# Kernel optimization log

Measured on AMD Instinct MI355X. Metric: run time of the kernel, lower is better.

## Reference

```python
import jax, jax.numpy as jnp
import numpy as np

N = 50000        # nodes per type (MiRNA=0, Disease=1, LncRNA=2)
E = 500000       # edges per relation
F_IN, HID, OUT = 128, 64, 64
ITEMS, SIZE, T = 4096, 4096, 100
# relation order: MvsD, DvsM, MvsL, LvsM, LvsD, DvsL
SRC = (0, 1, 0, 2, 2, 1)
DST = (1, 0, 2, 0, 1, 2)


def _sage_hetero_layer(h, edges, Wp, bp, Ws, bs, Wn):
    """One HeteroGraphConv(SAGEConv pool, aggregate='sum') layer.
    h: list of 3 [N, Fin] node-feature arrays; edges: [6, 2, E] int."""
    n = h[0].shape[0]
    out = [None, None, None]
    for e in range(6):
        s, d = SRC[e], DST[e]
        pooled = jax.nn.relu(h[s] @ Wp[e] + bp[e])                 # [N, Fin]
        msg = pooled[edges[e, 0]]                                  # [E, Fin] gather at src
        agg = jax.ops.segment_max(msg, edges[e, 1], num_segments=n)
        agg = jnp.where(jnp.isneginf(agg), 0.0, agg)               # DGL: 0 for isolated dst
        o = h[d] @ Ws[e] + bs[e] + agg @ Wn[e]                     # fc_self(+bias) + fc_neigh
        out[d] = o if out[d] is None else out[d] + o
    return out


def setup_inputs() -> dict:
    key = jax.random.key(0)
    ks = jax.random.split(key, 32)
    s = 0.05
    inp = {
        'hM': jax.random.normal(ks[0], (N, F_IN), jnp.float32),
        'hD': jax.random.normal(ks[1], (N, F_IN), jnp.float32),
        'hL': jax.random.normal(ks[2], (N, F_IN), jnp.float32),
        'Wpool1': jax.random.normal(ks[3], (6, F_IN, F_IN), jnp.float32) * s,
        'bpool1': jnp.zeros((6, F_IN), jnp.float32),
        'Wself1': jax.random.normal(ks[4], (6, F_IN, HID), jnp.float32) * s,
        'bself1': jnp.zeros((6, HID), jnp.float32),
        'Wneigh1': jax.random.normal(ks[5], (6, F_IN, HID), jnp.float32) * s,
        'Wpool2': jax.random.normal(ks[6], (6, HID, HID), jnp.float32) * s,
        'bpool2': jnp.zeros((6, HID), jnp.float32),
        'Wself2': jax.random.normal(ks[7], (6, HID, HID), jnp.float32) * s,
        'bself2': jnp.zeros((6, HID), jnp.float32),
        'Wneigh2': jax.random.normal(ks[8], (6, HID, HID), jnp.float32) * s,
        'Wpool3': jax.random.normal(ks[9], (6, HID, HID), jnp.float32) * s,
        'bpool3': jnp.zeros((6, HID), jnp.float32),
        'Wself3': jax.random.normal(ks[10], (6, HID, OUT), jnp.float32) * s,
        'bself3': jnp.zeros((6, OUT), jnp.float32),
        'Wneigh3': jax.random.normal(ks[11], (6, HID, OUT), jnp.float32) * s,
        'Adj': jax.random.uniform(ks[12], (SIZE, ITEMS), jnp.float32),
        'noise': jax.random.normal(ks[13], (N, OUT), jnp.float32),
        'W1': jax.random.normal(ks[14], (ITEMS + OUT, 256), jnp.float32) * s,
        'b1': jnp.zeros((256,), jnp.float32),
        'W2': jax.random.normal(ks[15], (256, 512), jnp.float32) * s,
        'b2': jnp.zeros((512,), jnp.float32),
        'W3': jax.random.normal(ks[16], (512, 1024), jnp.float32) * s,
        'b3': jnp.zeros((1024,), jnp.float32),
        'W4': jax.random.normal(ks[17], (1024, ITEMS), jnp.float32) * s,
        'b4': jnp.zeros((ITEMS,), jnp.float32),
        'edges': jax.random.randint(ks[18], (6, 2, E), 0, N, jnp.int32),
        't': 50,
        'size': SIZE,
        'leftIndex': 0,
    }
    return inp


def reference(hM, hD, hL, Wpool1, bpool1, Wself1, bself1, Wneigh1,
              Wpool2, bpool2, Wself2, bself2, Wneigh2,
              Wpool3, bpool3, Wself3, bself3, Wneigh3,
              Adj, noise, W1, b1, W2, b2, W3, b3, W4, b4,
              edges, t, size, leftIndex):
    h1 = _sage_hetero_layer([hM, hD, hL], edges, Wpool1, bpool1, Wself1, bself1, Wneigh1)
    h2 = _sage_hetero_layer(h1, edges, Wpool2, bpool2, Wself2, bself2, Wneigh2)
    h3 = _sage_hetero_layer(h2, edges, Wpool3, bpool3, Wself3, bself3, Wneigh3)
    mirna = h3[0]                                                  # [N, OUT]
    mirna = mirna / jnp.maximum(jnp.sum(jnp.abs(mirna), axis=1, keepdims=True), 1e-12)
    # diffusion schedule
    betas = jnp.linspace(1e-4, 0.02, T, dtype=jnp.float32)
    alpha_bars = jnp.cumprod(1.0 - betas)
    signal_rates = jnp.sqrt(alpha_bars)
    noise_rates = jnp.sqrt(1.0 - alpha_bars)
    noisy = signal_rates[t] * mirna + noise_rates[t] * noise
    fake = jax.lax.stop_gradient(noisy[leftIndex:leftIndex + size])  # detach + slice
    M = jnp.concatenate([Adj, fake], axis=1)                       # [size, ITEMS+OUT]
    x = jax.nn.relu(M @ W1 + b1)
    x = jax.nn.relu(x @ W2 + b2)
    x = jax.nn.relu(x @ W3 + b3)
    x = jax.nn.sigmoid(x @ W4 + b4)
    return fake, x
```

## Files before the change

### kernel.cpp

```cpp
#include <hip/hip_runtime.h>
#include <hip/hip_bf16.h>

#define NNODE 50000
#define NEDGE 500000
#define SZ    4096
#define NBKT  256
#define BWID  196
#define BCAP  4096
#define RELEB ((size_t)NBKT * BCAP)
#define ZK1   8

typedef __attribute__((ext_vector_type(8))) short bf16x8;
typedef __attribute__((ext_vector_type(4))) float f32x4;

__device__ __forceinline__ float bits2f(unsigned short u) {
    return __uint_as_float(((unsigned)u) << 16);
}
__device__ __forceinline__ unsigned short f2bits(float f) {
    unsigned x = __float_as_uint(f);
    unsigned r = x + 0x7fffu + ((x >> 16) & 1u);
    return (unsigned short)(r >> 16);
}
__device__ __forceinline__ unsigned pk_max_u16(unsigned a, unsigned b) {
    unsigned lo = max(a & 0xffffu, b & 0xffffu);
    unsigned hi = max(a >> 16, b >> 16);
    return lo | (hi << 16);
}
__device__ __forceinline__ void gl_lds16(const void* g, void* l) {
    __builtin_amdgcn_global_load_lds(
        (const __attribute__((address_space(1))) unsigned int*)g,
        (__attribute__((address_space(3))) unsigned int*)l, 16, 0, 0);
}

template<int RELU, int SIG, int OUTF32, int PART, int PIPE>
__global__ __launch_bounds__(256)
void gemm128(const unsigned short* __restrict__ A, const unsigned short* __restrict__ Bt,
             const float* __restrict__ bias, void* __restrict__ Cv, int M, int N, int K)
{
    __shared__ unsigned short As[PIPE + 1][128 * 64];
    __shared__ unsigned short Bs[PIPE + 1][128 * 64];
    const int tid = threadIdx.x;
    const int wave = tid >> 6, lane = tid & 63;
    const int m16 = lane & 15, quad = lane >> 4;
    const int wr = wave >> 1, wc = wave & 1;
    const int nwg = gridDim.x * gridDim.y;
    int bid = blockIdx.y * gridDim.x + blockIdx.x;
    if ((nwg & 7) == 0) { int cpx = nwg >> 3; bid = (bid & 7) * cpx + (bid >> 3); }
    const int bx = bid % gridDim.x, by = bid / gridDim.x;
    const int row0 = by * 128, col0 = bx * 128;
    const int lrow = lane >> 3, lcol = (lane & 7) * 8;

    f32x4 acc[4][4] = {};

    int k0beg = 0, k0end = K;
    if (PART) {
        const int per = ((K >> 6) + gridDim.z - 1) / gridDim.z;
        k0beg = blockIdx.z * per * 64;
        k0end = min(K, k0beg + per * 64);
    }
    const int nt = (k0end - k0beg) >> 6;

    auto STAGE = [&](int b, int k0) {
#pragma unroll
        for (int i = 0; i < 4; ++i) {
            int chunk = wave * 4 + i;
            int row = chunk * 8 + lrow;
            gl_lds16(A  + (size_t)(row0 + row) * K + k0 + lcol, &As[b][chunk * 512]);
            gl_lds16(Bt + (size_t)(col0 + row) * K + k0 + lcol, &Bs[b][chunk * 512]);
        }
    };
    auto COMPUTE = [&](int b) {
#pragma unroll
        for (int ks = 0; ks < 2; ++ks) {
            bf16x8 a[4], bb[4];
#pragma unroll
            for (int mt = 0; mt < 4; ++mt)
                a[mt] = *(const bf16x8*)&As[b][(wr * 64 + mt * 16 + m16) * 64 + ks * 32 + quad * 8];
#pragma unroll
            for (int nt2 = 0; nt2 < 4; ++nt2)
                bb[nt2] = *(const bf16x8*)&Bs[b][(wc * 64 + nt2 * 16 + m16) * 64 + ks * 32 + quad * 8];
#pragma unroll
            for (int mt = 0; mt < 4; ++mt)
#pragma unroll
                for (int nt2 = 0; nt2 < 4; ++nt2)
                    acc[mt][nt2] = __builtin_amdgcn_mfma_f32_16x16x32_bf16(a[mt], bb[nt2], acc[mt][nt2], 0, 0, 0);
        }
    };

    if (PIPE) {
        STAGE(0, k0beg);
        __syncthreads();
        int cur = 0;
        for (int t = 0; t < nt; ++t) {
            if (t + 1 < nt) STAGE(cur ^ 1, k0beg + (t + 1) * 64);
            COMPUTE(cur);
            __syncthreads();
            cur ^= 1;
        }
    } else {
        for (int t = 0; t < nt; ++t) {
            STAGE(0, k0beg + t * 64);
            __syncthreads();
            COMPUTE(0);
            __syncthreads();
        }
    }

    if (PART) {
        float* P = (float*)Cv + (size_t)blockIdx.z * M * N;
#pragma unroll
        for (int mt = 0; mt < 4; ++mt)
#pragma unroll
            for (int nt2 = 0; nt2 < 4; ++nt2) {
                int gc = col0 + wc * 64 + nt2 * 16 + m16;
#pragma unroll
                for (int r = 0; r < 4; ++r) {
                    int gm = row0 + wr * 64 + mt * 16 + quad * 4 + r;
                    P[(size_t)gm * N + gc] = acc[mt][nt2][r];
                }
            }
        return;
    }

#pragma unroll
    for (int mt = 0; mt < 4; ++mt) {
#pragma unroll
        for (int nt2 = 0; nt2 < 4; ++nt2) {
            int gc = col0 + wc * 64 + nt2 * 16 + m16;
            float bv = bias[gc];
#pragma unroll
            for (int r = 0; r < 4; ++r) {
                int gm = row0 + wr * 64 + mt * 16 + quad * 4 + r;
                size_t idx = (size_t)gm * N + gc;
                float v = acc[mt][nt2][r] + bv;
                if (RELU) v = fmaxf(v, 0.f);
                if (SIG)  v = 1.f / (1.f + __expf(-v));
                if (OUTF32) ((float*)Cv)[idx] = v;
                else        ((unsigned short*)Cv)[idx] = f2bits(v);
            }
        }
    }
}

__global__ __launch_bounds__(256)
void mlp1_ep_k(const float* __restrict__ p, const float* __restrict__ b1,
               unsigned short* __restrict__ x1)
{
    const size_t MN = (size_t)SZ * 256;
    int i = blockIdx.x * 256 + threadIdx.x;
    if (i >= (int)(MN / 4)) return;
    float4 s = ((const float4*)p)[i];
#pragma unroll
    for (int z = 1; z < ZK1; ++z) {
        float4 a = ((const float4*)(p + (size_t)z * MN))[i];
        s.x += a.x; s.y += a.y; s.z += a.z; s.w += a.w;
    }
    int base = i * 4;
    ushort4 o;
    o.x = f2bits(fmaxf(s.x + b1[(base + 0) & 255], 0.f));
    o.y = f2bits(fmaxf(s.y + b1[(base + 1) & 255], 0.f));
    o.z = f2bits(fmaxf(s.z + b1[(base + 2) & 255], 0.f));
    o.w = f2bits(fmaxf(s.w + b1[(base + 3) & 255], 0.f));
    ((ushort4*)x1)[i] = o;
}

template<int NT>
__global__ __launch_bounds__(256)
void pool2_k(const unsigned short* __restrict__ A0, const unsigned short* __restrict__ A1,
             const unsigned short* __restrict__ Bt0, const unsigned short* __restrict__ Bt1,
             const float* __restrict__ b0, const float* __restrict__ b1,
             unsigned short* __restrict__ out, int M, int K)
{
    __shared__ unsigned short As[64][72];
    __shared__ unsigned short Bs[NT * 16][72];
    const int z = blockIdx.z;
    const unsigned short* A = z ? A1 : A0;
    const unsigned short* Bt = z ? Bt1 : Bt0;
    const float* bias = z ? b1 : b0;
    const int N = NT * 16;
    unsigned short* Cv = out + (size_t)z * M * N;

    const int tid = threadIdx.x;
    const int wave = tid >> 6, lane = tid & 63;
    const int m16 = lane & 15, quad = lane >> 4;
    const int row0 = blockIdx.y * 64, col0 = blockIdx.x * N;

    f32x4 acc[NT] = {};

    for (int k0 = 0; k0 < K; k0 += 64) {
#pragma unroll
        for (int it = 0; it < 2; ++it) {
            int u = tid + it * 256;
            int m = u >> 3, c = (u & 7) * 8;
            int gm = row0 + m;
            uint4 v = make_uint4(0u, 0u, 0u, 0u);
            if (gm < M) v = *(const uint4*)(A + (size_t)gm * K + k0 + c);
            *(uint4*)&As[m][c] = v;
        }
#pragma unroll
        for (int it = 0; it < NT / 2; ++it) {
            int u = tid + it * 256;
            int n = u >> 3, c = (u & 7) * 8;
            uint4 v = *(const uint4*)(Bt + (size_t)(col0 + n) * K + k0 + c);
            *(uint4*)&Bs[n][c] = v;
        }
        __syncthreads();
#pragma unroll
        for (int ks = 0; ks < 2; ++ks) {
            bf16x8 a = *(const bf16x8*)&As[wave * 16 + m16][ks * 32 + quad * 8];
#pragma unroll
            for (int nt = 0; nt < NT; ++nt) {
                bf16x8 b = *(const bf16x8*)&Bs[nt * 16 + m16][ks * 32 + quad * 8];
                acc[nt] = __builtin_amdgcn_mfma_f32_16x16x32_bf16(a, b, acc[nt], 0, 0, 0);
            }
        }
        __syncthreads();
    }

#pragma unroll
    for (int nt = 0; nt < NT; ++nt) {
        int gc = col0 + nt * 16 + m16;
        float bv = bias[gc];
#pragma unroll
        for (int r = 0; r < 4; ++r) {
            int gm = row0 + wave * 16 + quad * 4 + r;
            if (gm < M)
                Cv[(size_t)gm * N + gc] = f2bits(fmaxf(acc[nt][r] + bv, 0.f));
        }
    }
}

__global__ __launch_bounds__(256)
void pool6_k(const unsigned short* __restrict__ hin, const unsigned short* __restrict__ pT,
             const float* __restrict__ bp, unsigned short* __restrict__ pooled6, int M)
{
    const int SRCr[6] = {0, 1, 0, 2, 2, 1};
    __shared__ unsigned short As[64][72];
    __shared__ unsigned short Bs[64][72];
    const int z = blockIdx.z;
    const unsigned short* A = hin + (size_t)SRCr[z] * M * 64;
    const unsigned short* Bt = pT + (size_t)z * 4096;
    const float* bias = bp + z * 64;
    unsigned short* Cv = pooled6 + (size_t)z * M * 64;

    const int tid = threadIdx.x;
    const int wave = tid >> 6, lane = tid & 63;
    const int m16 = lane & 15, quad = lane >> 4;
    const int row0 = blockIdx.y * 64;

    f32x4 acc[4] = {};

    {
#pragma unroll
        for (int it = 0; it < 2; ++it) {
            int u = tid + it * 256;
            int m = u >> 3, c = (u & 7) * 8;
            int gm = row0 + m;
            uint4 v = make_uint4(0u, 0u, 0u, 0u);
            if (gm < M) v = *(const uint4*)(A + (size_t)gm * 64 + c);
            *(uint4*)&As[m][c] = v;
        }
#pragma unroll
        for (int it = 0; it < 2; ++it) {
            int u = tid + it * 256;
            int n = u >> 3, c = (u & 7) * 8;
            uint4 v = *(const uint4*)(Bt + (size_t)n * 64 + c);
            *(uint4*)&Bs[n][c] = v;
        }
        __syncthreads();
#pragma unroll
        for (int ks = 0; ks < 2; ++ks) {
            bf16x8 a = *(const bf16x8*)&As[wave * 16 + m16][ks * 32 + quad * 8];
#pragma unroll
            for (int nt = 0; nt < 4; ++nt) {
                bf16x8 b = *(const bf16x8*)&Bs[nt * 16 + m16][ks * 32 + quad * 8];
                acc[nt] = __builtin_amdgcn_mfma_f32_16x16x32_bf16(a, b, acc[nt], 0, 0, 0);
            }
        }
    }

#pragma unroll
    for (int nt = 0; nt < 4; ++nt) {
        int gc = nt * 16 + m16;
        float bv = bias[gc];
#pragma unroll
        for (int r = 0; r < 4; ++r) {
            int gm = row0 + wave * 16 + quad * 4 + r;
            if (gm < M)
                Cv[(size_t)gm * 64 + gc] = f2bits(fmaxf(acc[nt][r] + bv, 0.f));
        }
    }
}

template<int NT>
__global__ __launch_bounds__(256)
void mfma_gemm(const unsigned short* __restrict__ A1, const unsigned short* __restrict__ A2,
               const unsigned short* __restrict__ A3,
               const unsigned short* __restrict__ Bt, const float* __restrict__ bias,
               const float* __restrict__ bias2,
               unsigned short* __restrict__ Cv, int M, int N, int Ka, int Kb, int Kc)
{
    __shared__ unsigned short As[64][72];
    __shared__ unsigned short Bs[NT * 16][72];
    const int tid = threadIdx.x;
    const int wave = tid >> 6, lane = tid & 63;
    const int m16 = lane & 15, quad = lane >> 4;
    const int row0 = blockIdx.y * 64, col0 = blockIdx.x * (NT * 16);
    const int K = Ka + Kb + Kc;

    f32x4 acc[NT] = {};

    for (int k0 = 0; k0 < K; k0 += 64) {
        const int seg = (k0 >= Ka + Kb) ? 2 : ((k0 >= Ka) ? 1 : 0);
        const unsigned short* src = seg == 2 ? A3 : (seg == 1 ? A2 : A1);
        const int ld = seg == 2 ? Kc : (seg == 1 ? Kb : Ka);
        const int kb = k0 - (seg == 2 ? Ka + Kb : (seg == 1 ? Ka : 0));
#pragma unroll
        for (int it = 0; it < 2; ++it) {
            int u = tid + it * 256;
            int m = u >> 3, c = (u & 7) * 8;
            int gm = row0 + m;
            uint4 v = make_uint4(0u, 0u, 0u, 0u);
            if (gm < M) v = *(const uint4*)(src + (size_t)gm * ld + kb + c);
            *(uint4*)&As[m][c] = v;
        }
#pragma unroll
        for (int it = 0; it < NT / 2; ++it) {
            int u = tid + it * 256;
            int n = u >> 3, c = (u & 7) * 8;
            uint4 v = *(const uint4*)(Bt + (size_t)(col0 + n) * K + k0 + c);
            *(uint4*)&Bs[n][c] = v;
        }
        __syncthreads();
#pragma unroll
        for (int ks = 0; ks < 2; ++ks) {
            bf16x8 a = *(const bf16x8*)&As[wave * 16 + m16][ks * 32 + quad * 8];
#pragma unroll
            for (int nt = 0; nt < NT; ++nt) {
                bf16x8 b = *(const bf16x8*)&Bs[nt * 16 + m16][ks * 32 + quad * 8];
                acc[nt] = __builtin_amdgcn_mfma_f32_16x16x32_bf16(a, b, acc[nt], 0, 0, 0);
            }
        }
        __syncthreads();
    }

#pragma unroll
    for (int nt = 0; nt < NT; ++nt) {
        int gc = col0 + nt * 16 + m16;
        float bv = bias[gc] + bias2[gc];
#pragma unroll
        for (int r = 0; r < 4; ++r) {
            int gm = row0 + wave * 16 + quad * 4 + r;
            if (gm < M)
                Cv[(size_t)gm * N + gc] = f2bits(acc[nt][r] + bv);
        }
    }
}

__global__ __launch_bounds__(256)
void fused3_k(const unsigned short* __restrict__ hin,
              const unsigned short* __restrict__ regA, const unsigned short* __restrict__ regB,
              const unsigned short* __restrict__ fT, const float* __restrict__ bs,
              unsigned short* __restrict__ hout, int M)
{
    const int PAe[3] = {1, 0, 2}, PBe[3] = {3, 4, 5};
    __shared__ unsigned short As[64][72];
    __shared__ unsigned short Bs[64][72];
    const int z = blockIdx.z;
    const int eA = PAe[z], eB = PBe[z];
    const unsigned short* A1 = hin + (size_t)z * M * 64;
    const unsigned short* A2 = (eA < 4) ? regA + (size_t)eA * M * 64 : regB + (size_t)(eA - 4) * M * 64;
    const unsigned short* A3 = (eB < 4) ? regA + (size_t)eB * M * 64 : regB + (size_t)(eB - 4) * M * 64;
    const unsigned short* Bt = fT + (size_t)z * 12288;
    const float* bias = bs + eA * 64;
    const float* bias2 = bs + eB * 64;
    unsigned short* Cv = hout + (size_t)z * M * 64;

    const int tid = threadIdx.x;
    const int wave = tid >> 6, lane = tid & 63;
    const int m16 = lane & 15, quad = lane >> 4;
    const int row0 = blockIdx.y * 64;

    f32x4 acc[4] = {};

#pragma unroll
    for (int seg = 0; seg < 3; ++seg) {
        const unsigned short* src = seg == 2 ? A3 : (seg == 1 ? A2 : A1);
        const int k0 = seg * 64;
#pragma unroll
        for (int it = 0; it < 2; ++it) {
            int u = tid + it * 256;
            int m = u >> 3, c = (u & 7) * 8;
            int gm = row0 + m;
            uint4 v = make_uint4(0u, 0u, 0u, 0u);
            if (gm < M) v = *(const uint4*)(src + (size_t)gm * 64 + c);
            *(uint4*)&As[m][c] = v;
        }
#pragma unroll
        for (int it = 0; it < 2; ++it) {
            int u = tid + it * 256;
            int n = u >> 3, c = (u & 7) * 8;
            uint4 v = *(const uint4*)(Bt + (size_t)n * 192 + k0 + c);
            *(uint4*)&Bs[n][c] = v;
        }
        __syncthreads();
#pragma unroll
        for (int ks = 0; ks < 2; ++ks) {
            bf16x8 a = *(const bf16x8*)&As[wave * 16 + m16][ks * 32 + quad * 8];
#pragma unroll
            for (int nt = 0; nt < 4; ++nt) {
                bf16x8 b = *(const bf16x8*)&Bs[nt * 16 + m16][ks * 32 + quad * 8];
                acc[nt] = __builtin_amdgcn_mfma_f32_16x16x32_bf16(a, b, acc[nt], 0, 0, 0);
            }
        }
        __syncthreads();
    }

#pragma unroll
    for (int nt = 0; nt < 4; ++nt) {
        int gc = nt * 16 + m16;
        float bv = bias[gc] + bias2[gc];
#pragma unroll
        for (int r = 0; r < 4; ++r) {
            int gm = row0 + wave * 16 + quad * 4 + r;
            if (gm < M)
                Cv[(size_t)gm * 64 + gc] = f2bits(acc[nt][r] + bv);
        }
    }
}

__global__ __launch_bounds__(256)
void transpose_cvt(const float* __restrict__ src1, const float* __restrict__ src2,
                   unsigned short* __restrict__ dst, int R1, int R2, int Nn)
{
    __shared__ float tile[32][33];
    const int R = R1 + R2;
    const int e = blockIdx.z;
    src1 += (size_t)e * R1 * Nn;
    if (src2) src2 += (size_t)e * R2 * Nn;
    dst += (size_t)e * Nn * R;
    const int r0 = blockIdx.x * 32, n0 = blockIdx.y * 32;
    const int lr = threadIdx.x >> 5, ln = threadIdx.x & 31;
#pragma unroll
    for (int i = 0; i < 4; ++i) {
        int r = r0 + lr + i * 8, n = n0 + ln;
        float v = 0.f;
        if (r < R && n < Nn) v = (r < R1) ? src1[(size_t)r * Nn + n]
                                          : src2[(size_t)(r - R1) * Nn + n];
        tile[lr + i * 8][ln] = v;
    }
    __syncthreads();
#pragma unroll
    for (int i = 0; i < 4; ++i) {
        int n = n0 + lr + i * 8, r = r0 + ln;
        if (n < Nn && r < R) dst[(size_t)n * R + r] = f2bits(tile[ln][lr + i * 8]);
    }
}

__global__ __launch_bounds__(256)
void fuse_w_k(const float* __restrict__ Ws, const float* __restrict__ Wn,
              unsigned short* __restrict__ dst, int F)
{
    const int PAe[3] = {1, 0, 2}, PBe[3] = {3, 4, 5};
    __shared__ float tile[32][33];
    const int p = blockIdx.z;
    const int eA = PAe[p], eB = PBe[p];
    const int Kt = 3 * F;
    unsigned short* D = dst + (size_t)p * 64 * Kt;
    const int r0 = blockIdx.x * 32;
    const int n0 = blockIdx.y * 32;
    const int lr = threadIdx.x >> 5, ln = threadIdx.x & 31;
    for (int seg = 0; seg < 3; ++seg) {
        __syncthreads();
#pragma unroll
        for (int i = 0; i < 4; ++i) {
            int r = r0 + lr + i * 8, n = n0 + ln;
            float v;
            if (seg == 0)
                v = Ws[((size_t)eA * F + r) * 64 + n] + Ws[((size_t)eB * F + r) * 64 + n];
            else if (seg == 1)
                v = Wn[((size_t)eA * F + r) * 64 + n];
            else
                v = Wn[((size_t)eB * F + r) * 64 + n];
            tile[lr + i * 8][ln] = v;
        }
        __syncthreads();
        const int koff = seg * F;
#pragma unroll
        for (int i = 0; i < 4; ++i) {
            int n = n0 + lr + i * 8, r = r0 + ln;
            D[(size_t)n * Kt + koff + r] = f2bits(tile[ln][lr + i * 8]);
        }
    }
}

__global__ __launch_bounds__(256)
void cvt3_k(const float* __restrict__ s0, const float* __restrict__ s1,
            const float* __restrict__ s2, unsigned short* __restrict__ dst)
{
    const int z = blockIdx.z;
    const float* src = z == 0 ? s0 : (z == 1 ? s1 : s2);
    dst += (size_t)z * NNODE * 128;
    int i = blockIdx.x * 256 + threadIdx.x;
    if (i >= 1600000) return;
    float4 v = ((const float4*)src)[i];
    ushort4 w;
    w.x = f2bits(v.x); w.y = f2bits(v.y); w.z = f2bits(v.z); w.w = f2bits(v.w);
    ((ushort4*)dst)[i] = w;
}

__global__ __launch_bounds__(256)
void cvt_adj_k(const float* __restrict__ src, unsigned short* __restrict__ dst)
{
    int i = blockIdx.x * 256 + threadIdx.x;
    if (i >= 4194304) return;
    int r = i >> 10, c4 = i & 1023;
    float4 v = ((const float4*)src)[i];
    ushort4 w;
    w.x = f2bits(v.x); w.y = f2bits(v.y); w.z = f2bits(v.z); w.w = f2bits(v.w);
    *(ushort4*)(dst + (size_t)r * 4160 + c4 * 4) = w;
}

__global__ __launch_bounds__(256)
void binit_k(int* __restrict__ bcur)
{
    bcur[blockIdx.x * NBKT + threadIdx.x] = threadIdx.x * BCAP;
}

__global__ __launch_bounds__(256)
void bucket_k(const int* __restrict__ edges, int* __restrict__ bcur,
              unsigned* __restrict__ ebuf)
{
    const int r = blockIdx.y;
    const int base = blockIdx.x * 4096;
    const int tid = threadIdx.x;
    __shared__ int lcnt[NBKT];
    __shared__ int lbase[NBKT];
    for (int i = tid; i < NBKT; i += 256) lcnt[i] = 0;
    __syncthreads();
    unsigned ent[16];
    int rnk[16];
#pragma unroll
    for (int i = 0; i < 16; ++i) {
        int e = base + tid + i * 256;
        ent[i] = 0xffffffffu;
        rnk[i] = 0;
        if (e < NEDGE) {
            int src = edges[(size_t)r * 2 * NEDGE + e];
            int dst = edges[(size_t)r * 2 * NEDGE + NEDGE + e];
            ent[i] = ((unsigned)dst << 16) | (unsigned)src;
            rnk[i] = atomicAdd(&lcnt[dst / BWID], 1);
        }
    }
    __syncthreads();
    for (int i = tid; i < NBKT; i += 256)
        lbase[i] = lcnt[i] ? atomicAdd(&bcur[r * NBKT + i], lcnt[i]) : 0;
    __syncthreads();
#pragma unroll
    for (int i = 0; i < 16; ++i)
        if (ent[i] != 0xffffffffu) {
            int b = (int)(ent[i] >> 16) / BWID;
            int pos = lbase[b] + rnk[i];
            if (pos < (b + 1) * BCAP)
                ebuf[(size_t)r * RELEB + pos] = ent[i];
        }
}

__global__ __launch_bounds__(256)
void bscan_k(const int* __restrict__ bcur, int* __restrict__ bbase,
             int* __restrict__ offs)
{
    const int r = blockIdx.x, tid = threadIdx.x;
    const int lane = tid & 63, wv = tid >> 6;
    int v = bcur[r * NBKT + tid] - tid * BCAP;
    if (v > BCAP) v = BCAP;
    int x = v;
#pragma unroll
    for (int off = 1; off < 64; off <<= 1) {
        int t = __shfl_up(x, off);
        if (lane >= off) x += t;
    }
    __shared__ int wsum[4];
    if (lane == 63) wsum[wv] = x;
    __syncthreads();
    int add = 0;
#pragma unroll
    for (int w = 0; w < 4; ++w) if (w < wv) add += wsum[w];
    x += add;
    bbase[r * NBKT + tid] = x - v;
    if (tid == 255) offs[(size_t)r * (NNODE + 1) + NNODE] = x;
}

__global__ __launch_bounds__(256)
void debucket_k(const unsigned* __restrict__ ebuf, const int* __restrict__ bcur,
                const int* __restrict__ bbase, int* __restrict__ offs,
                unsigned short* __restrict__ srcs)
{
    const int r = blockIdx.y, b = blockIdx.x, tid = threadIdx.x;
    const int lo = b * BWID;
    __shared__ unsigned es[BCAP];
    __shared__ unsigned short stage[BCAP];
    __shared__ int lhist[256];
    __shared__ int buf[256];
    __shared__ int lcur[256];
    int cnt = bcur[r * NBKT + b] - b * BCAP;
    if (cnt > BCAP) cnt = BCAP;
    const int base = bbase[r * NBKT + b];
    lhist[tid] = 0;
    __syncthreads();
    for (int j = tid; j < cnt; j += 256) {
        unsigned e = ebuf[(size_t)r * RELEB + (size_t)b * BCAP + j];
        es[j] = e;
        atomicAdd(&lhist[(int)(e >> 16) - lo], 1);
    }
    __syncthreads();
    int v = lhist[tid];
    buf[tid] = v;
    __syncthreads();
    for (int off = 1; off < 256; off <<= 1) {
        int t = (tid >= off) ? buf[tid - off] : 0;
        __syncthreads();
        buf[tid] += t;
        __syncthreads();
    }
    int excl = buf[tid] - v;
    int node = lo + tid;
    if (tid < BWID && node < NNODE) offs[(size_t)r * (NNODE + 1) + node] = base + excl;
    lcur[tid] = excl;
    __syncthreads();
    for (int j = tid; j < cnt; j += 256) {
        unsigned e = es[j];
        int d = (int)(e >> 16) - lo;
        int p = atomicAdd(&lcur[d], 1);
        stage[p] = (unsigned short)(e & 0xffffu);
    }
    __syncthreads();
    for (int j = tid; j < cnt; j += 256)
        srcs[(size_t)r * NEDGE + base + j] = stage[j];
}

template<int F>
__global__ __launch_bounds__(256)
void gather2_k(const unsigned short* __restrict__ pooled, const int* __restrict__ offs,
               const unsigned short* __restrict__ srcs, unsigned short* __restrict__ agg,
               int e0, int e1)
{
    const int CG = F / 8;
    const int z = blockIdx.z;
    const int e = z ? e1 : e0;
    pooled += (size_t)z * NNODE * F;
    agg    += (size_t)z * NNODE * F;
    offs   += (size_t)e * (NNODE + 1);
    srcs   += (size_t)e * NEDGE;
    int idx = blockIdx.x * 256 + threadIdx.x;
    int n = idx / CG, cg = idx % CG;
    if (n >= NNODE) return;
    int beg = offs[n], end = offs[n + 1];
    unsigned m0 = 0, m1 = 0, m2 = 0, m3 = 0;
    int j = beg;
    for (; j + 4 <= end; j += 4) {
        int s0 = srcs[j], s1 = srcs[j + 1], s2 = srcs[j + 2], s3 = srcs[j + 3];
        uint4 v0 = *(const uint4*)(pooled + (size_t)s0 * F + cg * 8);
        uint4 v1 = *(const uint4*)(pooled + (size_t)s1 * F + cg * 8);
        uint4 v2 = *(const uint4*)(pooled + (size_t)s2 * F + cg * 8);
        uint4 v3 = *(const uint4*)(pooled + (size_t)s3 * F + cg * 8);
        m0 = pk_max_u16(m0, pk_max_u16(pk_max_u16(v0.x, v1.x), pk_max_u16(v2.x, v3.x)));
        m1 = pk_max_u16(m1, pk_max_u16(pk_max_u16(v0.y, v1.y), pk_max_u16(v2.y, v3.y)));
        m2 = pk_max_u16(m2, pk_max_u16(pk_max_u16(v0.z, v1.z), pk_max_u16(v2.z, v3.z)));
        m3 = pk_max_u16(m3, pk_max_u16(pk_max_u16(v0.w, v1.w), pk_max_u16(v2.w, v3.w)));
    }
    for (; j < end; ++j) {
        int s = srcs[j];
        uint4 v = *(const uint4*)(pooled + (size_t)s * F + cg * 8);
        m0 = pk_max_u16(m0, v.x);
        m1 = pk_max_u16(m1, v.y);
        m2 = pk_max_u16(m2, v.z);
        m3 = pk_max_u16(m3, v.w);
    }
    uint4 o; o.x = m0; o.y = m1; o.z = m2; o.w = m3;
    *(uint4*)(agg + (size_t)n * F + cg * 8) = o;
}

__global__ __launch_bounds__(256)
void gather6_k(const unsigned short* __restrict__ pooled6, const int* __restrict__ offs,
               const unsigned short* __restrict__ srcs,
               unsigned short* __restrict__ regA, unsigned short* __restrict__ regB)
{
    const int F = 64, CG = 8;
    const int z = blockIdx.z;
    const unsigned short* pooled = pooled6 + (size_t)z * NNODE * F;
    unsigned short* agg = (z < 4) ? regA + (size_t)z * NNODE * F
                                  : regB + (size_t)(z - 4) * NNODE * F;
    offs += (size_t)z * (NNODE + 1);
    srcs += (size_t)z * NEDGE;
    int idx = blockIdx.x * 256 + threadIdx.x;
    int n = idx / CG, cg = idx % CG;
    if (n >= NNODE) return;
    int beg = offs[n], end = offs[n + 1];
    unsigned m0 = 0, m1 = 0, m2 = 0, m3 = 0;
    int j = beg;
    for (; j + 4 <= end; j += 4) {
        int s0 = srcs[j], s1 = srcs[j + 1], s2 = srcs[j + 2], s3 = srcs[j + 3];
        uint4 v0 = *(const uint4*)(pooled + (size_t)s0 * F + cg * 8);
        uint4 v1 = *(const uint4*)(pooled + (size_t)s1 * F + cg * 8);
        uint4 v2 = *(const uint4*)(pooled + (size_t)s2 * F + cg * 8);
        uint4 v3 = *(const uint4*)(pooled + (size_t)s3 * F + cg * 8);
        m0 = pk_max_u16(m0, pk_max_u16(pk_max_u16(v0.x, v1.x), pk_max_u16(v2.x, v3.x)));
        m1 = pk_max_u16(m1, pk_max_u16(pk_max_u16(v0.y, v1.y), pk_max_u16(v2.y, v3.y)));
        m2 = pk_max_u16(m2, pk_max_u16(pk_max_u16(v0.z, v1.z), pk_max_u16(v2.z, v3.z)));
        m3 = pk_max_u16(m3, pk_max_u16(pk_max_u16(v0.w, v1.w), pk_max_u16(v2.w, v3.w)));
    }
    for (; j < end; ++j) {
        int s = srcs[j];
        uint4 v = *(const uint4*)(pooled + (size_t)s * F + cg * 8);
        m0 = pk_max_u16(m0, v.x);
        m1 = pk_max_u16(m1, v.y);
        m2 = pk_max_u16(m2, v.z);
        m3 = pk_max_u16(m3, v.w);
    }
    uint4 o; o.x = m0; o.y = m1; o.z = m2; o.w = m3;
    *(uint4*)(agg + (size_t)n * F + cg * 8) = o;
}

__global__ __launch_bounds__(64)
void fake_k(const unsigned short* __restrict__ mirna, const float* __restrict__ noise,
            const int* __restrict__ t_p, const int* __restrict__ left_p,
            unsigned short* __restrict__ adj_s, float* __restrict__ fake_out)
{
    int r = blockIdx.x, c = threadIdx.x;
    int t = *t_p, left = *left_p;
    int row = left + r;
    float x = bits2f(mirna[(size_t)row * 64 + c]);
    float s = fabsf(x);
#pragma unroll
    for (int off = 32; off > 0; off >>= 1) s += __shfl_down(s, off);
    s = __shfl(s, 0);
    float ab = 1.f;
    for (int i = 0; i <= t; ++i)
        ab *= (1.f - (1e-4f + (0.02f - 1e-4f) * ((float)i / 99.f)));
    float v = sqrtf(ab) * (x / fmaxf(s, 1e-12f)) + sqrtf(1.f - ab) * noise[(size_t)row * 64 + c];
    adj_s[(size_t)r * 4160 + 4096 + c] = f2bits(v);
    fake_out[(size_t)r * 64 + c] = v;
}

extern "C" void kernel_launch(void* const* d_in, const int* in_sizes, int n_in,
                              void* d_out, int out_size, void* d_ws, size_t ws_size,
                              hipStream_t stream)
{
    const float* h0[3]    = {(const float*)d_in[0], (const float*)d_in[1], (const float*)d_in[2]};
    const float* Wpool[3] = {(const float*)d_in[3], (const float*)d_in[8],  (const float*)d_in[13]};
    const float* bpool[3] = {(const float*)d_in[4], (const float*)d_in[9],  (const float*)d_in[14]};
    const float* bself[3] = {(const float*)d_in[6], (const float*)d_in[11], (const float*)d_in[16]};
    const float* Wself[3] = {(const float*)d_in[5], (const float*)d_in[10], (const float*)d_in[15]};
    const float* Wneigh[3]= {(const float*)d_in[7], (const float*)d_in[12], (const float*)d_in[17]};
    const float* Adj   = (const float*)d_in[18];
    const float* noise = (const float*)d_in[19];
    const float* W1 = (const float*)d_in[20]; const float* b1 = (const float*)d_in[21];
    const float* W2 = (const float*)d_in[22]; const float* b2 = (const float*)d_in[23];
    const float* W3 = (const float*)d_in[24]; const float* b3 = (const float*)d_in[25];
    const float* W4 = (const float*)d_in[26]; const float* b4 = (const float*)d_in[27];
    const int* edges  = (const int*)d_in[28];
    const int* t_p    = (const int*)d_in[29];
    const int* left_p = (const int*)d_in[31];

    unsigned short* ws = (unsigned short*)d_ws;
    const size_t P1 = 0, P2 = 98304, P3 = 122880;
    const size_t FU1 = 147456, FU2 = 245760, FU3 = 294912;
    const size_t W1T = 344064, W2T = 1409024, W3T = 1540096, W4T = 2064384;
    const size_t ADJ = 6258688;
    const size_t POOLED = 23298048;
    const size_t HA = 36098048, HB = 45698048;
    int* bcur  = (int*)(ws + 55298048);
    int* bbase = bcur + 6 * NBKT;
    int* offs  = bbase + 6 * NBKT;
    unsigned short* srcs = (unsigned short*)(offs + 6 * (NNODE + 1));
    unsigned* ebuf = (unsigned*)(ws + POOLED);
    unsigned short* x1 = ws + POOLED;
    unsigned short* x2 = x1 + (size_t)SZ * 256;
    unsigned short* x3 = x2 + (size_t)SZ * 512;
    unsigned short* adj_s = ws + ADJ;
    float* out_fake = (float*)d_out;
    float* out_x    = out_fake + (size_t)SZ * 64;
    unsigned short* hb0 = (unsigned short*)out_x;
    unsigned short* agg2_l1 = hb0 + 19200000;
    unsigned short* pooled6 = (unsigned short*)out_x;
    unsigned short* aggB6 = pooled6 + 19200000;
    unsigned short* aggA6 = ws + POOLED;
    float* x1p = out_x;

    const int SRCr[6] = {0, 1, 0, 2, 2, 1};
    const int PAe[3] = {1, 0, 2}, PBe[3] = {3, 4, 5};
    dim3 T(256);

    transpose_cvt<<<dim3(4, 4, 6),   T, 0, stream>>>(Wpool[0], nullptr, ws + P1, 128, 0, 128);
    transpose_cvt<<<dim3(2, 2, 6),   T, 0, stream>>>(Wpool[1], nullptr, ws + P2, 64, 0, 64);
    transpose_cvt<<<dim3(2, 2, 6),   T, 0, stream>>>(Wpool[2], nullptr, ws + P3, 64, 0, 64);
    fuse_w_k<<<dim3(4, 2, 3), T, 0, stream>>>(Wself[0], Wneigh[0], ws + FU1, 128);
    fuse_w_k<<<dim3(2, 2, 3), T, 0, stream>>>(Wself[1], Wneigh[1], ws + FU2, 64);
    fuse_w_k<<<dim3(2, 2, 3), T, 0, stream>>>(Wself[2], Wneigh[2], ws + FU3, 64);
    transpose_cvt<<<dim3(130, 8, 1), T, 0, stream>>>(W1, nullptr, ws + W1T, 4160, 0, 256);
    transpose_cvt<<<dim3(8, 16, 1),  T, 0, stream>>>(W2, nullptr, ws + W2T, 256, 0, 512);
    transpose_cvt<<<dim3(16, 32, 1), T, 0, stream>>>(W3, nullptr, ws + W3T, 512, 0, 1024);
    transpose_cvt<<<dim3(32, 128, 1),T, 0, stream>>>(W4, nullptr, ws + W4T, 1024, 0, 4096);
    cvt_adj_k<<<16384, T, 0, stream>>>(Adj, adj_s);
    cvt3_k<<<dim3(6250, 1, 3), T, 0, stream>>>(h0[0], h0[1], h0[2], hb0);

    binit_k<<<6, T, 0, stream>>>(bcur);
    bucket_k<<<dim3(123, 6), T, 0, stream>>>(edges, bcur, ebuf);
    bscan_k<<<6, T, 0, stream>>>(bcur, bbase, offs);
    debucket_k<<<dim3(NBKT, 6), T, 0, stream>>>(ebuf, bcur, bbase, offs, srcs);

    for (int p = 0; p < 3; ++p) {
        const int eA = PAe[p], eB = PBe[p];
        pool2_k<8><<<dim3(1, 782, 2), T, 0, stream>>>(
            hb0 + (size_t)SRCr[eA] * NNODE * 128, hb0 + (size_t)SRCr[eB] * NNODE * 128,
            ws + P1 + (size_t)eA * 16384, ws + P1 + (size_t)eB * 16384,
            bpool[0] + eA * 128, bpool[0] + eB * 128,
            ws + POOLED, NNODE, 128);
        gather2_k<128><<<dim3(3125, 1, 2), T, 0, stream>>>(
            ws + POOLED, offs, srcs, agg2_l1, eA, eB);
        mfma_gemm<4><<<dim3(1, 782), T, 0, stream>>>(
            hb0 + (size_t)p * NNODE * 128, agg2_l1, agg2_l1 + (size_t)NNODE * 128,
            ws + FU1 + (size_t)p * 24576, bself[0] + eA * 64, bself[0] + eB * 64,
            ws + HA + (size_t)p * NNODE * 64, NNODE, 64, 128, 128, 128);
    }

    unsigned short* hin = ws + HA;
    unsigned short* hout = ws + HB;
    for (int layer = 1; layer <= 2; ++layer) {
        const unsigned short* pT = ws + (layer == 1 ? P2 : P3);
        const unsigned short* fT = ws + (layer == 1 ? FU2 : FU3);
        pool6_k<<<dim3(1, 782, 6), T, 0, stream>>>(hin, pT, bpool[layer], pooled6, NNODE);
        gather6_k<<<dim3(1563, 1, 6), T, 0, stream>>>(pooled6, offs, srcs, aggA6, aggB6);
        fused3_k<<<dim3(1, 782, 3), T, 0, stream>>>(hin, aggA6, aggB6, fT,
                                                    bself[layer], hout, NNODE);
        unsigned short* tmp = hin; hin = hout; hout = tmp;
    }

    fake_k<<<SZ, dim3(64), 0, stream>>>(hin, noise, t_p, left_p, adj_s, out_fake);

    gemm128<0, 0, 0, 1, 1><<<dim3(2, 32, ZK1), T, 0, stream>>>(
        adj_s, ws + W1T, b1, x1p, SZ, 256, 4160);
    mlp1_ep_k<<<1024, T, 0, stream>>>(x1p, b1, x1);
    gemm128<1, 0, 0, 0, 1><<<dim3(4, 32),  T, 0, stream>>>(x1, ws + W2T, b2, x2, SZ, 512, 256);
    gemm128<1, 0, 0, 0, 1><<<dim3(8, 32),  T, 0, stream>>>(x2, ws + W3T, b3, x3, SZ, 1024, 512);
    gemm128<0, 1, 1, 0, 0><<<dim3(32, 32), T, 0, stream>>>(x3, ws + W4T, b4, out_x, SZ, 4096, 1024);
}
```

Baseline: 884.8 us.

## Sort destination nodes by degree for gather load balance; batch weight conversions

Adds a counting sort of destination nodes by in-degree (histogram, scan, fill) per relation and makes the gather kernels process nodes in that order. Neighbouring threads in a wave then have similar loop trip counts, which cuts divergence in the segment-max loops. It also merges several small weight transpose/fuse launches into fewer kernels to reduce launch overhead. The cost is three extra preprocessing kernels and gather writes that are no longer in node order, so stores scatter.

```diff
diff --git a/kernel.cpp b/kernel.cpp
--- a/kernel.cpp
+++ b/kernel.cpp
@@ -431,22 +431,55 @@
 
 __global__ __launch_bounds__(256)
 void transpose_cvt(const float* __restrict__ src1, const float* __restrict__ src2,
-                   unsigned short* __restrict__ dst, int R1, int R2, int Nn)
+                   unsigned short* __restrict__ dst, int R1, int R2, int Nn,
+                   const float* __restrict__ src1b, unsigned short* __restrict__ dstb)
 {
     __shared__ float tile[32][33];
     const int R = R1 + R2;
-    const int e = blockIdx.z;
-    src1 += (size_t)e * R1 * Nn;
-    if (src2) src2 += (size_t)e * R2 * Nn;
-    dst += (size_t)e * Nn * R;
+    int e = blockIdx.z;
+    const float* s1 = src1;
+    unsigned short* d = dst;
+    if (src1b && e >= 6) { s1 = src1b; d = dstb; e -= 6; }
+    s1 += (size_t)e * R1 * Nn;
+    const float* s2 = src2 ? src2 + (size_t)e * R2 * Nn : nullptr;
+    d += (size_t)e * Nn * R;
     const int r0 = blockIdx.x * 32, n0 = blockIdx.y * 32;
     const int lr = threadIdx.x >> 5, ln = threadIdx.x & 31;
 #pragma unroll
     for (int i = 0; i < 4; ++i) {
         int r = r0 + lr + i * 8, n = n0 + ln;
         float v = 0.f;
-        if (r < R && n < Nn) v = (r < R1) ? src1[(size_t)r * Nn + n]
-                                          : src2[(size_t)(r - R1) * Nn + n];
+        if (r < R && n < Nn) v = (r < R1) ? s1[(size_t)r * Nn + n]
+                                          : s2[(size_t)(r - R1) * Nn + n];
+        tile[lr + i * 8][ln] = v;
+    }
+    __syncthreads();
+#pragma unroll
+    for (int i = 0; i < 4; ++i) {
+        int n = n0 + lr + i * 8, r = r0 + ln;
+        if (n < Nn && r < R) d[(size_t)n * R + r] = f2bits(tile[ln][lr + i * 8]);
+    }
+}
+
+__global__ __launch_bounds__(256)
+void tcvt_mlp_k(const float* __restrict__ W2, const float* __restrict__ W3,
+                const float* __restrict__ W4, unsigned short* __restrict__ d2,
+                unsigned short* __restrict__ d3, unsigned short* __restrict__ d4)
+{
+    const int z = blockIdx.z;
+    const float* src; unsigned short* dst; int R, Nn, gx, gy;
+    if (z == 0)      { src = W2; dst = d2; R = 256;  Nn = 512;  gx = 8;  gy = 16; }
+    else if (z == 1) { src = W3; dst = d3; R = 512;  Nn = 1024; gx = 16; gy = 32; }
+    else             { src = W4; dst = d4; R = 1024; Nn = 4096; gx = 32; gy = 128; }
+    if (blockIdx.x >= (unsigned)gx || blockIdx.y >= (unsigned)gy) return;
+    __shared__ float tile[32][33];
+    const int r0 = blockIdx.x * 32, n0 = blockIdx.y * 32;
+    const int lr = threadIdx.x >> 5, ln = threadIdx.x & 31;
+#pragma unroll
+    for (int i = 0; i < 4; ++i) {
+        int r = r0 + lr + i * 8, n = n0 + ln;
+        float v = 0.f;
+        if (r < R && n < Nn) v = src[(size_t)r * Nn + n];
         tile[lr + i * 8][ln] = v;
     }
     __syncthreads();
@@ -459,14 +492,18 @@
 
 __global__ __launch_bounds__(256)
 void fuse_w_k(const float* __restrict__ Ws, const float* __restrict__ Wn,
-              unsigned short* __restrict__ dst, int F)
+              unsigned short* __restrict__ dst, int F,
+              const float* __restrict__ Wsb, const float* __restrict__ Wnb,
+              unsigned short* __restrict__ dstb)
 {
     const int PAe[3] = {1, 0, 2}, PBe[3] = {3, 4, 5};
     __shared__ float tile[32][33];
-    const int p = blockIdx.z;
+    int p = blockIdx.z;
+    const float* ws_ = Ws; const float* wn_ = Wn; unsigned short* db = dst;
+    if (Wsb && p >= 3) { ws_ = Wsb; wn_ = Wnb; db = dstb; p -= 3; }
     const int eA = PAe[p], eB = PBe[p];
     const int Kt = 3 * F;
-    unsigned short* D = dst + (size_t)p * 64 * Kt;
+    unsigned short* D = db + (size_t)p * 64 * Kt;
     const int r0 = blockIdx.x * 32;
     const int n0 = blockIdx.y * 32;
     const int lr = threadIdx.x >> 5, ln = threadIdx.x & 31;
@@ -477,11 +514,11 @@
             int r = r0 + lr + i * 8, n = n0 + ln;
             float v;
             if (seg == 0)
-                v = Ws[((size_t)eA * F + r) * 64 + n] + Ws[((size_t)eB * F + r) * 64 + n];
+                v = ws_[((size_t)eA * F + r) * 64 + n] + ws_[((size_t)eB * F + r) * 64 + n];
             else if (seg == 1)
-                v = Wn[((size_t)eA * F + r) * 64 + n];
+                v = wn_[((size_t)eA * F + r) * 64 + n];
             else
-                v = Wn[((size_t)eB * F + r) * 64 + n];
+                v = wn_[((size_t)eB * F + r) * 64 + n];
             tile[lr + i * 8][ln] = v;
         }
         __syncthreads();
@@ -522,9 +559,10 @@
 }
 
 __global__ __launch_bounds__(256)
-void binit_k(int* __restrict__ bcur)
+void binit_k(int* __restrict__ bcur, int* __restrict__ dh)
 {
     bcur[blockIdx.x * NBKT + threadIdx.x] = threadIdx.x * BCAP;
+    if (threadIdx.x < 64) dh[blockIdx.x * 64 + threadIdx.x] = 0;
 }
 
 __global__ __launch_bounds__(256)
@@ -639,11 +677,66 @@
         srcs[(size_t)r * NEDGE + base + j] = stage[j];
 }
 
+__global__ __launch_bounds__(256)
+void dhist_k(const int* __restrict__ offs, int* __restrict__ dh)
+{
+    const int r = blockIdx.y;
+    const int n = blockIdx.x * 256 + threadIdx.x;
+    __shared__ int h[64];
+    if (threadIdx.x < 64) h[threadIdx.x] = 0;
+    __syncthreads();
+    if (n < NNODE) {
+        int d = offs[(size_t)r * (NNODE + 1) + n + 1] - offs[(size_t)r * (NNODE + 1) + n];
+        atomicAdd(&h[min(d, 63)], 1);
+    }
+    __syncthreads();
+    if (threadIdx.x < 64 && h[threadIdx.x])
+        atomicAdd(&dh[r * 64 + threadIdx.x], h[threadIdx.x]);
+}
+
+__global__ __launch_bounds__(64)
+void dscan_k(int* __restrict__ dh)
+{
+    const int r = blockIdx.x, t = threadIdx.x;
+    int v = dh[r * 64 + t];
+    int x = v;
+#pragma unroll
+    for (int off = 1; off < 64; off <<= 1) {
+        int u = __shfl_up(x, off);
+        if (t >= off) x += u;
+    }
+    dh[r * 64 + t] = x - v;
+}
+
+__global__ __launch_bounds__(256)
+void dfill_k(const int* __restrict__ offs, int* __restrict__ dcur,
+             unsigned short* __restrict__ order)
+{
+    const int r = blockIdx.y;
+    const int n = blockIdx.x * 256 + threadIdx.x;
+    const int tid = threadIdx.x;
+    __shared__ int lcnt[64];
+    __shared__ int lbase[64];
+    if (tid < 64) lcnt[tid] = 0;
+    __syncthreads();
+    int bin = 0, rnk = 0;
+    bool ok = n < NNODE;
+    if (ok) {
+        int d = offs[(size_t)r * (NNODE + 1) + n + 1] - offs[(size_t)r * (NNODE + 1) + n];
+        bin = min(d, 63);
+        rnk = atomicAdd(&lcnt[bin], 1);
+    }
+    __syncthreads();
+    if (tid < 64) lbase[tid] = lcnt[tid] ? atomicAdd(&dcur[r * 64 + tid], lcnt[tid]) : 0;
+    __syncthreads();
+    if (ok) order[(size_t)r * NNODE + lbase[bin] + rnk] = (unsigned short)n;
+}
+
 template<int F>
 __global__ __launch_bounds__(256)
 void gather2_k(const unsigned short* __restrict__ pooled, const int* __restrict__ offs,
-               const unsigned short* __restrict__ srcs, unsigned short* __restrict__ agg,
-               int e0, int e1)
+               const unsigned short* __restrict__ srcs, const unsigned short* __restrict__ order,
+               unsigned short* __restrict__ agg, int e0, int e1)
 {
     const int CG = F / 8;
     const int z = blockIdx.z;
@@ -652,9 +745,11 @@
     agg    += (size_t)z * NNODE * F;
     offs   += (size_t)e * (NNODE + 1);
     srcs   += (size_t)e * NEDGE;
+    order  += (size_t)e * NNODE;
     int idx = blockIdx.x * 256 + threadIdx.x;
-    int n = idx / CG, cg = idx % CG;
-    if (n >= NNODE) return;
+    int g = idx / CG, cg = idx % CG;
+    if (g >= NNODE) return;
+    int n = order[g];
     int beg = offs[n], end = offs[n + 1];
     unsigned m0 = 0, m1 = 0, m2 = 0, m3 = 0;
     int j = beg;
@@ -683,7 +778,7 @@
 
 __global__ __launch_bounds__(256)
 void gather6_k(const unsigned short* __restrict__ pooled6, const int* __restrict__ offs,
-               const unsigned short* __restrict__ srcs,
+               const unsigned short* __restrict__ srcs, const unsigned short* __restrict__ order,
                unsigned short* __restrict__ regA, unsigned short* __restrict__ regB)
 {
     const int F = 64, CG = 8;
@@ -691,11 +786,13 @@
     const unsigned short* pooled = pooled6 + (size_t)z * NNODE * F;
     unsigned short* agg = (z < 4) ? regA + (size_t)z * NNODE * F
                                   : regB + (size_t)(z - 4) * NNODE * F;
-    offs += (size_t)z * (NNODE + 1);
-    srcs += (size_t)z * NEDGE;
+    offs  += (size_t)z * (NNODE + 1);
+    srcs  += (size_t)z * NEDGE;
+    order += (size_t)z * NNODE;
     int idx = blockIdx.x * 256 + threadIdx.x;
-    int n = idx / CG, cg = idx % CG;
-    if (n >= NNODE) return;
+    int g = idx / CG, cg = idx % CG;
+    if (g >= NNODE) return;
+    int n = order[g];
     int beg = offs[n], end = offs[n + 1];
     unsigned m0 = 0, m1 = 0, m2 = 0, m3 = 0;
     int j = beg;
@@ -773,7 +870,9 @@
     int* bcur  = (int*)(ws + 55298048);
     int* bbase = bcur + 6 * NBKT;
     int* offs  = bbase + 6 * NBKT;
-    unsigned short* srcs = (unsigned short*)(offs + 6 * (NNODE + 1));
+    int* dh    = offs + 6 * (NNODE + 1);
+    unsigned short* srcs = (unsigned short*)(dh + 6 * 64);
+    unsigned short* order = srcs + (size_t)6 * NEDGE;
     unsigned* ebuf = (unsigned*)(ws + POOLED);
     unsigned short* x1 = ws + POOLED;
     unsigned short* x2 = x1 + (size_t)SZ * 256;
@@ -792,23 +891,27 @@
     const int PAe[3] = {1, 0, 2}, PBe[3] = {3, 4, 5};
     dim3 T(256);
 
-    transpose_cvt<<<dim3(4, 4, 6),   T, 0, stream>>>(Wpool[0], nullptr, ws + P1, 128, 0, 128);
-    transpose_cvt<<<dim3(2, 2, 6),   T, 0, stream>>>(Wpool[1], nullptr, ws + P2, 64, 0, 64);
-    transpose_cvt<<<dim3(2, 2, 6),   T, 0, stream>>>(Wpool[2], nullptr, ws + P3, 64, 0, 64);
-    fuse_w_k<<<dim3(4, 2, 3), T, 0, stream>>>(Wself[0], Wneigh[0], ws + FU1, 128);
-    fuse_w_k<<<dim3(2, 2, 3), T, 0, stream>>>(Wself[1], Wneigh[1], ws + FU2, 64);
-    fuse_w_k<<<dim3(2, 2, 3), T, 0, stream>>>(Wself[2], Wneigh[2], ws + FU3, 64);
-    transpose_cvt<<<dim3(130, 8, 1), T, 0, stream>>>(W1, nullptr, ws + W1T, 4160, 0, 256);
-    transpose_cvt<<<dim3(8, 16, 1),  T, 0, stream>>>(W2, nullptr, ws + W2T, 256, 0, 512);
-    transpose_cvt<<<dim3(16, 32, 1), T, 0, stream>>>(W3, nullptr, ws + W3T, 512, 0, 1024);
-    transpose_cvt<<<dim3(32, 128, 1),T, 0, stream>>>(W4, nullptr, ws + W4T, 1024, 0, 4096);
+    transpose_cvt<<<dim3(4, 4, 6), T, 0, stream>>>(Wpool[0], nullptr, ws + P1, 128, 0, 128,
+                                                   nullptr, nullptr);
+    transpose_cvt<<<dim3(2, 2, 12), T, 0, stream>>>(Wpool[1], nullptr, ws + P2, 64, 0, 64,
+                                                    Wpool[2], ws + P3);
+    fuse_w_k<<<dim3(4, 2, 3), T, 0, stream>>>(Wself[0], Wneigh[0], ws + FU1, 128,
+                                              nullptr, nullptr, nullptr);
+    fuse_w_k<<<dim3(2, 2, 6), T, 0, stream>>>(Wself[1], Wneigh[1], ws + FU2, 64,
+                                              Wself[2], Wneigh[2], ws + FU3);
+    transpose_cvt<<<dim3(130, 8, 1), T, 0, stream>>>(W1, nullptr, ws + W1T, 4160, 0, 256,
+                                                     nullptr, nullptr);
+    tcvt_mlp_k<<<dim3(32, 128, 3), T, 0, stream>>>(W2, W3, W4, ws + W2T, ws + W3T, ws + W4T);
     cvt_adj_k<<<16384, T, 0, stream>>>(Adj, adj_s);
     cvt3_k<<<dim3(6250, 1, 3), T, 0, stream>>>(h0[0], h0[1], h0[2], hb0);
 
-    binit_k<<<6, T, 0, stream>>>(bcur);
+    binit_k<<<6, T, 0, stream>>>(bcur, dh);
     bucket_k<<<dim3(123, 6), T, 0, stream>>>(edges, bcur, ebuf);
     bscan_k<<<6, T, 0, stream>>>(bcur, bbase, offs);
     debucket_k<<<dim3(NBKT, 6), T, 0, stream>>>(ebuf, bcur, bbase, offs, srcs);
+    dhist_k<<<dim3(196, 6), T, 0, stream>>>(offs, dh);
+    dscan_k<<<6, dim3(64), 0, stream>>>(dh);
+    dfill_k<<<dim3(196, 6), T, 0, stream>>>(offs, dh, order);
 
     for (int p = 0; p < 3; ++p) {
         const int eA = PAe[p], eB = PBe[p];
@@ -818,7 +921,7 @@
             bpool[0] + eA * 128, bpool[0] + eB * 128,
             ws + POOLED, NNODE, 128);
         gather2_k<128><<<dim3(3125, 1, 2), T, 0, stream>>>(
-            ws + POOLED, offs, srcs, agg2_l1, eA, eB);
+            ws + POOLED, offs, srcs, order, agg2_l1, eA, eB);
         mfma_gemm<4><<<dim3(1, 782), T, 0, stream>>>(
             hb0 + (size_t)p * NNODE * 128, agg2_l1, agg2_l1 + (size_t)NNODE * 128,
             ws + FU1 + (size_t)p * 24576, bself[0] + eA * 64, bself[0] + eB * 64,
@@ -831,7 +934,7 @@
         const unsigned short* pT = ws + (layer == 1 ? P2 : P3);
         const unsigned short* fT = ws + (layer == 1 ? FU2 : FU3);
         pool6_k<<<dim3(1, 782, 6), T, 0, stream>>>(hin, pT, bpool[layer], pooled6, NNODE);
-        gather6_k<<<dim3(1563, 1, 6), T, 0, stream>>>(pooled6, offs, srcs, aggA6, aggB6);
+        gather6_k<<<dim3(1563, 1, 6), T, 0, stream>>>(pooled6, offs, srcs, order, aggA6, aggB6);
         fused3_k<<<dim3(1, 782, 3), T, 0, stream>>>(hin, aggA6, aggB6, fT,
                                                     bself[layer], hout, NNODE);
         unsigned short* tmp = hin; hin = hout; hout = tmp;
```

New measurement: 881.6 us. About the same (-0.4%).
